# Performance work log

Hardware: AMD Instinct MI355X
Metric: run time of the kernel (lower is better)

The kernel has to match this reference:

```python
import jax, jax.numpy as jnp
import numpy as np

B, D_CAT, C_IN, C_OUT, K, H, W = 16, 512, 256, 256, 3, 64, 64


def setup_inputs() -> dict:
    key = jax.random.key(0)
    ks = jax.random.split(key, 9)
    inp = {
        "x": jax.random.normal(ks[0], (B, C_IN, H, W), dtype=jnp.float32),
        "y": jax.random.normal(ks[1], (B, D_CAT), dtype=jnp.float32),
        # EqualLinear stack: d_catin -> in_channels, then n_dl=2 layers in_channels -> in_channels
        "w0": jax.random.normal(ks[2], (C_IN, D_CAT), dtype=jnp.float32) / np.sqrt(D_CAT),
        "b0": jnp.zeros((C_IN,), dtype=jnp.float32),
        "w1": jax.random.normal(ks[3], (C_IN, C_IN), dtype=jnp.float32) / np.sqrt(C_IN),
        "b1": jnp.zeros((C_IN,), dtype=jnp.float32),
        "w2": jax.random.normal(ks[4], (C_IN, C_IN), dtype=jnp.float32) / np.sqrt(C_IN),
        "b2": jnp.zeros((C_IN,), dtype=jnp.float32),
        # shared conv weight (O, I, k, k), modulated per sample
        "conv_w": jax.random.normal(ks[5], (C_OUT, C_IN, K, K), dtype=jnp.float32) / np.sqrt(C_IN * K * K),
    }
    return inp


def _lrelu(z):
    # nn.LeakyReLU default negative_slope = 0.01
    return jnp.where(z >= 0, z, 0.01 * z)


def reference(x, y, w0, b0, w1, b1, w2, b2, conv_w):
    # style MLP (EqualLinear stack with LeakyReLU)
    s = _lrelu(y @ w0.T + b0)          # (B, C_in)
    s = _lrelu(s @ w1.T + b1)
    s = _lrelu(s @ w2.T + b2)
    # Per-sample weight modulation: conv(x[b], W * s[b, None, :, None, None]).
    # Since the scale is per input channel (no demodulation), this is exactly
    # equivalent to scaling the input channels and running one shared conv —
    # the fused form a custom kernel would use.
    x_mod = x * s[:, :, None, None]    # (B, C_in, H, W)
    out = jax.lax.conv_general_dilated(
        x_mod, conv_w,
        window_strides=(1, 1),
        padding=((1, 1), (1, 1)),
        dimension_numbers=("NCHW", "OIHW", "NCHW"),
    )  # (B, C_out, H, W); conv has bias=False in _DyConv
    return out
```

## Files before the change

### kernel.cpp

```cpp
#include <hip/hip_runtime.h>

typedef short bf16x8 __attribute__((ext_vector_type(8)));
typedef float f32x4 __attribute__((ext_vector_type(4)));
typedef unsigned short ushort8 __attribute__((ext_vector_type(8)));
typedef unsigned short ushort4v __attribute__((ext_vector_type(4)));

#define BATCH 16
#define DCAT 512
#define CIN 256
#define COUT 256
#define HH 64
#define WW 64
#define HP 66
#define WP 66
#define PLANE (HP * WP * 8)
#define AHALO 52224
#define BBUF 32768

__device__ __forceinline__ unsigned short f2bf(float f) {
  unsigned int u = __float_as_uint(f);
  unsigned int r = (u + 0x7fffu + ((u >> 16) & 1u)) >> 16;
  return (unsigned short)r;
}

template <int IN_DIM>
__global__ void __launch_bounds__(256) mlp_layer(const float* __restrict__ in,
                                                 const float* __restrict__ w,
                                                 const float* __restrict__ bias,
                                                 float* __restrict__ out) {
  int wid = threadIdx.x >> 6, lane = threadIdx.x & 63;
  int oidx = blockIdx.x * 4 + wid;
  int b = oidx >> 8, c = oidx & 255;
  const float* wr = w + (size_t)c * IN_DIM;
  const float* ir = in + (size_t)b * IN_DIM;
  float sum = 0.f;
#pragma unroll
  for (int d0 = 0; d0 < IN_DIM; d0 += 256) {
    f32x4 wv = *(const f32x4*)(wr + d0 + lane * 4);
    f32x4 iv = *(const f32x4*)(ir + d0 + lane * 4);
    sum += wv[0] * iv[0] + wv[1] * iv[1] + wv[2] * iv[2] + wv[3] * iv[3];
  }
#pragma unroll
  for (int off = 32; off; off >>= 1) sum += __shfl_xor(sum, off, 64);
  if (lane == 0) {
    float a = sum + bias[c];
    out[oidx] = a >= 0.f ? a : 0.01f * a;
  }
}

__global__ void __launch_bounds__(256) prep_all(const float* __restrict__ t1,
                                                const float* __restrict__ w2,
                                                const float* __restrict__ b2,
                                                const float* __restrict__ x,
                                                const float* __restrict__ cw,
                                                unsigned short* __restrict__ xpad,
                                                unsigned short* __restrict__ wt) {
  int blk = blockIdx.x;
  int tid = threadIdx.x;

  if (blk >= 1024) {
    int idx = (blk - 1024) * 256 + tid;
    int t = idx / 16384;
    int r = idx - t * 16384;
    int o = r >> 6, i4 = r & 63;
    ushort4v v;
#pragma unroll
    for (int j = 0; j < 4; j++) v[j] = f2bf(cw[(o * 256 + i4 * 4 + j) * 9 + t]);
    *(ushort4v*)(wt + ((size_t)(t * COUT + o)) * CIN + i4 * 4) = v;
    return;
  }

  int h = blk & 1, c8 = (blk >> 1) & 31, b = blk >> 6;
  int wid = tid >> 6, lane = tid & 63;

  float tv = t1[b * CIN + tid];
  float pj[8];
#pragma unroll
  for (int j = 0; j < 8; j++) pj[j] = w2[(size_t)(c8 * 8 + j) * CIN + tid] * tv;

  const float* xb = x + ((size_t)(b * CIN + c8 * 8)) * (HH * WW);
  int gg0 = h * 512 + tid;
  int gg1 = gg0 + 256;
  int hh0 = (gg0 >> 4) + 1, w00 = (gg0 & 15) * 4 + 1;
  int hh1 = (gg1 >> 4) + 1, w01 = (gg1 & 15) * 4 + 1;
  int base0 = (hh0 - 1) * WW + (w00 - 1);
  int base1 = (hh1 - 1) * WW + (w01 - 1);
  f32x4 v0[8], v1[8];
#pragma unroll
  for (int j = 0; j < 8; j++) v0[j] = *(const f32x4*)(xb + j * (HH * WW) + base0);
#pragma unroll
  for (int j = 0; j < 8; j++) v1[j] = *(const f32x4*)(xb + j * (HH * WW) + base1);

#pragma unroll
  for (int off = 32; off; off >>= 1)
#pragma unroll
    for (int j = 0; j < 8; j++) pj[j] += __shfl_xor(pj[j], off, 64);
  __shared__ float red[4][8];
  __shared__ float sv_sh[8];
  if (lane == 0)
#pragma unroll
    for (int j = 0; j < 8; j++) red[wid][j] = pj[j];
  __syncthreads();
  if (tid < 8) {
    float a = red[0][tid] + red[1][tid] + red[2][tid] + red[3][tid] + b2[c8 * 8 + tid];
    sv_sh[tid] = a >= 0.f ? a : 0.01f * a;
  }
  __syncthreads();
  float sv[8];
#pragma unroll
  for (int j = 0; j < 8; j++) sv[j] = sv_sh[j];

  unsigned short* xp = xpad + ((size_t)(b * 32 + c8)) * PLANE;

  if (tid < 130) {
    int i = h * 130 + tid;
    int bh, bw;
    if (i < 66) { bh = 0; bw = i; }
    else if (i < 132) { bh = 65; bw = i - 66; }
    else if (i < 196) { bh = i - 132 + 1; bw = 0; }
    else { bh = i - 196 + 1; bw = 65; }
    ushort8 z = {0, 0, 0, 0, 0, 0, 0, 0};
    *(ushort8*)(xp + (bh * WP + bw) * 8) = z;
  }

  unsigned short* op0 = xp + (hh0 * WP + w00) * 8;
  unsigned short* op1 = xp + (hh1 * WP + w01) * 8;
#pragma unroll
  for (int t2 = 0; t2 < 4; t2++) {
    ushort8 o;
#pragma unroll
    for (int j = 0; j < 8; j++) o[j] = f2bf(v0[j][t2] * sv[j]);
    *(ushort8*)(op0 + t2 * 8) = o;
  }
#pragma unroll
  for (int t2 = 0; t2 < 4; t2++) {
    ushort8 o;
#pragma unroll
    for (int j = 0; j < 8; j++) o[j] = f2bf(v1[j][t2] * sv[j]);
    *(ushort8*)(op1 + t2 * 8) = o;
  }
}

__device__ __forceinline__ void gl2lds16(const void* g, void* l) {
  __builtin_amdgcn_global_load_lds((const __attribute__((address_space(1))) void*)g,
                                   (__attribute__((address_space(3))) void*)l, 16, 0, 0);
}

__global__ void __launch_bounds__(512, 1) gemm_conv(const unsigned short* __restrict__ xpad,
                                                    const unsigned short* __restrict__ wt,
                                                    float* __restrict__ out) {
  __shared__ __align__(16) char lds[AHALO + 2 * BBUF];
  int tid = threadIdx.x;
  int wid = tid >> 6, lane = tid & 63;
  int bid = blockIdx.x;
  int m_t = (bid & 7) * 32 + (bid >> 3);
  int m0 = m_t << 8;
  int b = m0 >> 12;
  int h0 = (m0 >> 6) & 63;
  int wm = wid & 1, wn = wid >> 1;

  f32x4 acc[8][4];
#pragma unroll
  for (int mi = 0; mi < 8; mi++)
#pragma unroll
    for (int ni = 0; ni < 4; ni++) acc[mi][ni] = (f32x4){0.f, 0.f, 0.f, 0.f};

  const unsigned short* aSrc[7];
#pragma unroll
  for (int i = 0; i < 7; i++) {
    int c = (i * 8 + wid) * 64 + lane;
    int e = c >> 3, cs = c & 7;
    int gs = cs ^ (e & 7);
    int rh = e / 68, wc = e - rh * 68;
    aSrc[i] = xpad + ((size_t)((b * 32 + gs) * HP + (h0 + rh))) * (WP * 8) + wc * 8;
  }

  int o_l = tid >> 3;
  int csb = tid & 7;
  const unsigned short* bL = wt + o_l * CIN + ((csb ^ (o_l & 7)) * 8);

  int qa = lane >> 4;
  int l15 = lane & 15;
  int rB = wn * 64 + l15;
  int offB0 = rB * 128 + ((qa ^ (rB & 7)) * 16);
  int offB1 = rB * 128 + (((qa + 4) ^ (rB & 7)) * 16);

  int cur = 0;
  for (int kc2 = 0; kc2 < 4; kc2++) {
    size_t kofs = (size_t)kc2 * 8 * PLANE;
#pragma unroll
    for (int i = 0; i < 6; i++)
      gl2lds16(aSrc[i] + kofs, lds + (i * 8 + wid) * 1024);
    if (wid < 3) gl2lds16(aSrc[6] + kofs, lds + (48 + wid) * 1024);
    {
      const unsigned short* bG = bL + kc2 * 64;
      char* dB = lds + AHALO + cur * BBUF + wid * 1024;
#pragma unroll
      for (int q = 0; q < 4; q++) gl2lds16(bG + q * 64 * CIN, dB + q * 8192);
    }
    __syncthreads();

    for (int kh = 0; kh < 3; kh++) {
      for (int kw = 0; kw < 3; kw++) {
        int tap = kh * 3 + kw;
        if (tap < 8) {
          const unsigned short* bG = bL + (tap + 1) * (COUT * CIN) + kc2 * 64;
          char* dB = lds + AHALO + (cur ^ 1) * BBUF + wid * 1024;
#pragma unroll
          for (int q = 0; q < 4; q++) gl2lds16(bG + q * 64 * CIN, dB + q * 8192);
        }

        int eb = (wm * 2 + kh) * 68 + l15 + kw;
        int s0 = eb & 7, s1 = (eb + 4) & 7;
        int a00 = eb * 128 + ((qa ^ s0) * 16);
        int a01 = (eb + 68) * 128 + ((qa ^ s1) * 16);
        int a10 = eb * 128 + (((qa + 4) ^ s0) * 16);
        int a11 = (eb + 68) * 128 + (((qa + 4) ^ s1) * 16);
        const char* Bb = lds + AHALO + cur * BBUF;

#pragma unroll
        for (int kb = 0; kb < 2; kb++) {
          int oa0 = kb ? a10 : a00;
          int oa1 = kb ? a11 : a01;
          int ob = kb ? offB1 : offB0;
          bf16x8 av[8], bv[4];
#pragma unroll
          for (int mi = 0; mi < 4; mi++) {
            av[mi] = *(const bf16x8*)(lds + oa0 + mi * 2048);
            av[4 + mi] = *(const bf16x8*)(lds + oa1 + mi * 2048);
          }
#pragma unroll
          for (int ni = 0; ni < 4; ni++)
            bv[ni] = *(const bf16x8*)(Bb + ob + ni * 2048);
          __builtin_amdgcn_s_setprio(1);
#pragma unroll
          for (int mi = 0; mi < 8; mi++)
#pragma unroll
            for (int ni = 0; ni < 4; ni++)
              acc[mi][ni] = __builtin_amdgcn_mfma_f32_16x16x32_bf16(av[mi], bv[ni],
                                                                    acc[mi][ni], 0, 0, 0);
          __builtin_amdgcn_s_setprio(0);
        }

        __syncthreads();
        cur ^= 1;
      }
    }
  }

  int pixbase = m0 & 4095;
  int quad = lane >> 4;
  int col = lane & 15;
#pragma unroll
  for (int mi = 0; mi < 8; mi++) {
    int pm = pixbase + wm * 128 + mi * 16 + quad * 4;
#pragma unroll
    for (int ni = 0; ni < 4; ni++) {
      int on = wn * 64 + ni * 16 + col;
      float* op = out + ((size_t)(b * COUT + on) << 12) + pm;
      *(f32x4*)op = acc[mi][ni];
    }
  }
}

extern "C" void kernel_launch(void* const* d_in, const int* in_sizes, int n_in,
                              void* d_out, int out_size, void* d_ws, size_t ws_size,
                              hipStream_t stream) {
  const float* x = (const float*)d_in[0];
  const float* y = (const float*)d_in[1];
  const float* w0 = (const float*)d_in[2];
  const float* b0 = (const float*)d_in[3];
  const float* w1 = (const float*)d_in[4];
  const float* b1 = (const float*)d_in[5];
  const float* w2 = (const float*)d_in[6];
  const float* b2 = (const float*)d_in[7];
  const float* cw = (const float*)d_in[8];
  float* out = (float*)d_out;

  char* ws = (char*)d_ws;
  unsigned short* xpad = (unsigned short*)ws;
  unsigned short* wt = (unsigned short*)(ws + 35684352);
  float* t0 = (float*)(ws + 35684352 + 2359296);
  float* t1 = (float*)(ws + 35684352 + 2359296 + 16384);

  mlp_layer<DCAT><<<BATCH * CIN / 4, 256, 0, stream>>>(y, w0, b0, t0);
  mlp_layer<CIN><<<BATCH * CIN / 4, 256, 0, stream>>>(t0, w1, b1, t1);
  prep_all<<<1024 + 576, 256, 0, stream>>>(t1, w2, b2, x, cw, xpad, wt);
  gemm_conv<<<BATCH * HH * WW / 256, 512, 0, stream>>>(xpad, wt, out);
}
```

Baseline: 199.0 us.

## Prefetch next chunk's first weight tap and hoist all LDS fragment loads before MFMAs

The weight tile for tap 0 of the next input-channel chunk is now prefetched during the last tap of the current chunk, instead of being loaded synchronously at the start of each chunk. This removes an exposed global-to-LDS load before the barrier at chunk boundaries. Separately, both k-halves' A and B fragments are loaded from LDS up front, then all 64 MFMAs issue back to back, which lets LDS latency overlap with compute. The cost is higher VGPR pressure from the doubled fragment registers, which could lower occupancy or cause spills.

```diff
diff --git a/kernel.cpp b/kernel.cpp
--- a/kernel.cpp
+++ b/kernel.cpp
@@ -192,9 +192,9 @@
     for (int i = 0; i < 6; i++)
       gl2lds16(aSrc[i] + kofs, lds + (i * 8 + wid) * 1024);
     if (wid < 3) gl2lds16(aSrc[6] + kofs, lds + (48 + wid) * 1024);
-    {
-      const unsigned short* bG = bL + kc2 * 64;
-      char* dB = lds + AHALO + cur * BBUF + wid * 1024;
+    if (kc2 == 0) {
+      const unsigned short* bG = bL;
+      char* dB = lds + AHALO + wid * 1024;
 #pragma unroll
       for (int q = 0; q < 4; q++) gl2lds16(bG + q * 64 * CIN, dB + q * 8192);
     }
@@ -203,8 +203,10 @@
     for (int kh = 0; kh < 3; kh++) {
       for (int kw = 0; kw < 3; kw++) {
         int tap = kh * 3 + kw;
-        if (tap < 8) {
-          const unsigned short* bG = bL + (tap + 1) * (COUT * CIN) + kc2 * 64;
+        if (tap < 8 || kc2 < 3) {
+          const unsigned short* bG = (tap < 8)
+              ? bL + (tap + 1) * (COUT * CIN) + kc2 * 64
+              : bL + (kc2 + 1) * 64;
           char* dB = lds + AHALO + (cur ^ 1) * BBUF + wid * 1024;
 #pragma unroll
           for (int q = 0; q < 4; q++) gl2lds16(bG + q * 64 * CIN, dB + q * 8192);
@@ -218,29 +220,39 @@
         int a11 = (eb + 68) * 128 + (((qa + 4) ^ s1) * 16);
         const char* Bb = lds + AHALO + cur * BBUF;
 
-#pragma unroll
-        for (int kb = 0; kb < 2; kb++) {
-          int oa0 = kb ? a10 : a00;
-          int oa1 = kb ? a11 : a01;
-          int ob = kb ? offB1 : offB0;
-          bf16x8 av[8], bv[4];
-#pragma unroll
-          for (int mi = 0; mi < 4; mi++) {
-            av[mi] = *(const bf16x8*)(lds + oa0 + mi * 2048);
-            av[4 + mi] = *(const bf16x8*)(lds + oa1 + mi * 2048);
-          }
+        bf16x8 av[8], bv0[4], aw[8], bv1[4];
+#pragma unroll
+        for (int mi = 0; mi < 4; mi++) {
+          av[mi] = *(const bf16x8*)(lds + a00 + mi * 2048);
+          av[4 + mi] = *(const bf16x8*)(lds + a01 + mi * 2048);
+        }
+#pragma unroll
+        for (int ni = 0; ni < 4; ni++)
+          bv0[ni] = *(const bf16x8*)(Bb + offB0 + ni * 2048);
+
+#pragma unroll
+        for (int mi = 0; mi < 4; mi++) {
+          aw[mi] = *(const bf16x8*)(lds + a10 + mi * 2048);
+          aw[4 + mi] = *(const bf16x8*)(lds + a11 + mi * 2048);
+        }
+#pragma unroll
+        for (int ni = 0; ni < 4; ni++)
+          bv1[ni] = *(const bf16x8*)(Bb + offB1 + ni * 2048);
+
+        __builtin_amdgcn_s_setprio(1);
+#pragma unroll
+        for (int mi = 0; mi < 8; mi++)
 #pragma unroll
           for (int ni = 0; ni < 4; ni++)
-            bv[ni] = *(const bf16x8*)(Bb + ob + ni * 2048);
-          __builtin_amdgcn_s_setprio(1);
-#pragma unroll
-          for (int mi = 0; mi < 8; mi++)
-#pragma unroll
-            for (int ni = 0; ni < 4; ni++)
-              acc[mi][ni] = __builtin_amdgcn_mfma_f32_16x16x32_bf16(av[mi], bv[ni],
-                                                                    acc[mi][ni], 0, 0, 0);
-          __builtin_amdgcn_s_setprio(0);
-        }
+            acc[mi][ni] = __builtin_amdgcn_mfma_f32_16x16x32_bf16(av[mi], bv0[ni],
+                                                                  acc[mi][ni], 0, 0, 0);
+#pragma unroll
+        for (int mi = 0; mi < 8; mi++)
+#pragma unroll
+          for (int ni = 0; ni < 4; ni++)
+            acc[mi][ni] = __builtin_amdgcn_mfma_f32_16x16x32_bf16(aw[mi], bv1[ni],
+                                                                  acc[mi][ni], 0, 0, 0);
+        __builtin_amdgcn_s_setprio(0);
 
         __syncthreads();
         cur ^= 1;
```

Measured after the change: 241.1 us. +21.1%, slower.

## Double-buffer input halo per channel slice with per-wave private weight tiles

Applied to the files above, without the earlier changes.

Splits the channel reduction into 8 slices of 32 channels with a double-buffered A halo. The next slice's halo is prefetched during tap 7 of the current slice. Each wave now stages its own private B weight tile, so the per-tap block barrier is replaced by vmcnt waits, and only one barrier per slice remains. This aims to overlap global-to-LDS loads with MFMA work and cut synchronisation. The cost is more, smaller pipeline steps, a finer swizzle, and fragile hand-written vmcnt counts.

```diff
diff --git a/kernel.cpp b/kernel.cpp
--- a/kernel.cpp
+++ b/kernel.cpp
@@ -14,8 +14,8 @@
 #define HP 66
 #define WP 66
 #define PLANE (HP * WP * 8)
-#define AHALO 52224
-#define BBUF 32768
+#define ABUF 26624
+#define BBASE (2 * ABUF)
 
 __device__ __forceinline__ unsigned short f2bf(float f) {
   unsigned int u = __float_as_uint(f);
@@ -149,7 +149,7 @@
 __global__ void __launch_bounds__(512, 1) gemm_conv(const unsigned short* __restrict__ xpad,
                                                     const unsigned short* __restrict__ wt,
                                                     float* __restrict__ out) {
-  __shared__ __align__(16) char lds[AHALO + 2 * BBUF];
+  __shared__ __align__(16) char lds[BBASE + 8 * 8192];
   int tid = threadIdx.x;
   int wid = tid >> 6, lane = tid & 63;
   int bid = blockIdx.x;
@@ -165,85 +165,102 @@
 #pragma unroll
     for (int ni = 0; ni < 4; ni++) acc[mi][ni] = (f32x4){0.f, 0.f, 0.f, 0.f};
 
-  const unsigned short* aSrc[7];
-#pragma unroll
-  for (int i = 0; i < 7; i++) {
-    int c = (i * 8 + wid) * 64 + lane;
-    int e = c >> 3, cs = c & 7;
-    int gs = cs ^ (e & 7);
-    int rh = e / 68, wc = e - rh * 68;
-    aSrc[i] = xpad + ((size_t)((b * 32 + gs) * HP + (h0 + rh))) * (WP * 8) + wc * 8;
-  }
-
-  int o_l = tid >> 3;
-  int csb = tid & 7;
-  const unsigned short* bL = wt + o_l * CIN + ((csb ^ (o_l & 7)) * 8);
+  const unsigned short* aSrc[4];
+  {
+    int gsA = (lane & 3) ^ ((lane >> 3) & 3);
+#pragma unroll
+    for (int i = 0; i < 4; i++) {
+      int L = wid + i * 8;
+      int e = L * 16 + (lane >> 2);
+      int rh = e / 68, wc = e - rh * 68;
+      aSrc[i] = xpad + ((size_t)((b * 32 + gsA) * HP + (h0 + rh))) * (WP * 8) + wc * 8;
+    }
+  }
+
+  const unsigned short* bS0 =
+      wt + (size_t)(wn * 64 + (lane >> 2)) * CIN + ((lane & 3) ^ ((lane >> 3) & 3)) * 8;
+  char* myB = lds + BBASE + wid * 8192;
 
   int qa = lane >> 4;
   int l15 = lane & 15;
-  int rB = wn * 64 + l15;
-  int offB0 = rB * 128 + ((qa ^ (rB & 7)) * 16);
-  int offB1 = rB * 128 + (((qa + 4) ^ (rB & 7)) * 16);
-
-  int cur = 0;
-  for (int kc2 = 0; kc2 < 4; kc2++) {
-    size_t kofs = (size_t)kc2 * 8 * PLANE;
-#pragma unroll
-    for (int i = 0; i < 6; i++)
-      gl2lds16(aSrc[i] + kofs, lds + (i * 8 + wid) * 1024);
-    if (wid < 3) gl2lds16(aSrc[6] + kofs, lds + (48 + wid) * 1024);
-    {
-      const unsigned short* bG = bL + kc2 * 64;
-      char* dB = lds + AHALO + cur * BBUF + wid * 1024;
-#pragma unroll
-      for (int q = 0; q < 4; q++) gl2lds16(bG + q * 64 * CIN, dB + q * 8192);
-    }
-    __syncthreads();
-
+  int obr = l15 * 64 + ((qa ^ ((l15 >> 1) & 3)) * 16);
+
+#define STAGE_B(BUF, SRC)                                        \
+  do {                                                           \
+    char* dB_ = myB + (BUF) * 4096;                              \
+    const unsigned short* s_ = (SRC);                            \
+    _Pragma("unroll")                                            \
+    for (int g = 0; g < 4; g++)                                  \
+      gl2lds16(s_ + g * 16 * CIN, dB_ + g * 1024);               \
+  } while (0)
+
+#define STAGE_A(SL)                                              \
+  do {                                                           \
+    size_t ao_ = (size_t)(SL) * 4 * PLANE;                       \
+    char* dA_ = lds + ((SL) & 1) * ABUF;                         \
+    _Pragma("unroll")                                            \
+    for (int i = 0; i < 4; i++) {                                \
+      int L_ = wid + i * 8;                                      \
+      if (L_ < 26) gl2lds16(aSrc[i] + ao_, dA_ + L_ * 1024);     \
+    }                                                            \
+  } while (0)
+
+  STAGE_A(0);
+  STAGE_B(0, bS0);
+  asm volatile("s_waitcnt vmcnt(0)" ::: "memory");
+  __builtin_amdgcn_s_barrier();
+
+  int bcur = 0;
+  for (int slice = 0; slice < 8; slice++) {
+    const char* Ac = lds + (slice & 1) * ABUF;
     for (int kh = 0; kh < 3; kh++) {
       for (int kw = 0; kw < 3; kw++) {
-        int tap = kh * 3 + kw;
-        if (tap < 8) {
-          const unsigned short* bG = bL + (tap + 1) * (COUT * CIN) + kc2 * 64;
-          char* dB = lds + AHALO + (cur ^ 1) * BBUF + wid * 1024;
-#pragma unroll
-          for (int q = 0; q < 4; q++) gl2lds16(bG + q * 64 * CIN, dB + q * 8192);
+        int t = kh * 3 + kw;
+        if (t < 8) {
+          STAGE_B(bcur ^ 1, bS0 + (size_t)(t + 1) * (COUT * CIN) + slice * 32);
+        } else if (slice < 7) {
+          STAGE_B(bcur ^ 1, bS0 + (slice + 1) * 32);
         }
+        if (t == 7 && slice < 7) STAGE_A(slice + 1);
+
+        if (t < 8) {
+          asm volatile("s_waitcnt vmcnt(4)" ::: "memory");
+        } else if (slice < 7) {
+          asm volatile("s_waitcnt vmcnt(7)" ::: "memory");
+        } else {
+          asm volatile("s_waitcnt vmcnt(0)" ::: "memory");
+        }
 
         int eb = (wm * 2 + kh) * 68 + l15 + kw;
-        int s0 = eb & 7, s1 = (eb + 4) & 7;
-        int a00 = eb * 128 + ((qa ^ s0) * 16);
-        int a01 = (eb + 68) * 128 + ((qa ^ s1) * 16);
-        int a10 = eb * 128 + (((qa + 4) ^ s0) * 16);
-        int a11 = (eb + 68) * 128 + (((qa + 4) ^ s1) * 16);
-        const char* Bb = lds + AHALO + cur * BBUF;
-
-#pragma unroll
-        for (int kb = 0; kb < 2; kb++) {
-          int oa0 = kb ? a10 : a00;
-          int oa1 = kb ? a11 : a01;
-          int ob = kb ? offB1 : offB0;
-          bf16x8 av[8], bv[4];
-#pragma unroll
-          for (int mi = 0; mi < 4; mi++) {
-            av[mi] = *(const bf16x8*)(lds + oa0 + mi * 2048);
-            av[4 + mi] = *(const bf16x8*)(lds + oa1 + mi * 2048);
-          }
+        int e2 = eb + 68;
+        int a0 = eb * 64 + ((qa ^ ((eb >> 1) & 3)) * 16);
+        int a1 = e2 * 64 + ((qa ^ ((e2 >> 1) & 3)) * 16);
+        const char* Bb = myB + bcur * 4096;
+
+        bf16x8 av[8], bv[4];
+#pragma unroll
+        for (int mi = 0; mi < 4; mi++) {
+          av[mi] = *(const bf16x8*)(Ac + a0 + mi * 1024);
+          av[4 + mi] = *(const bf16x8*)(Ac + a1 + mi * 1024);
+        }
+#pragma unroll
+        for (int ni = 0; ni < 4; ni++)
+          bv[ni] = *(const bf16x8*)(Bb + obr + ni * 1024);
+
+        __builtin_amdgcn_s_setprio(1);
+#pragma unroll
+        for (int mi = 0; mi < 8; mi++)
 #pragma unroll
           for (int ni = 0; ni < 4; ni++)
-            bv[ni] = *(const bf16x8*)(Bb + ob + ni * 2048);
-          __builtin_amdgcn_s_setprio(1);
-#pragma unroll
-          for (int mi = 0; mi < 8; mi++)
-#pragma unroll
-            for (int ni = 0; ni < 4; ni++)
-              acc[mi][ni] = __builtin_amdgcn_mfma_f32_16x16x32_bf16(av[mi], bv[ni],
-                                                                    acc[mi][ni], 0, 0, 0);
-          __builtin_amdgcn_s_setprio(0);
+            acc[mi][ni] = __builtin_amdgcn_mfma_f32_16x16x32_bf16(av[mi], bv[ni],
+                                                                  acc[mi][ni], 0, 0, 0);
+        __builtin_amdgcn_s_setprio(0);
+
+        if (t == 8 && slice < 7) {
+          asm volatile("s_waitcnt vmcnt(0)" ::: "memory");
+          __builtin_amdgcn_s_barrier();
         }
-
-        __syncthreads();
-        cur ^= 1;
+        bcur ^= 1;
       }
     }
   }
```

New measurement: 213.1 us. 1.07x slower.

## Shrink conv GEMM tile to 128x128 with two workgroups per CU

Applied to the files above, without the earlier changes.

The implicit-GEMM conv moves from 512-thread workgroups covering 256 pixels by all 256 output channels to 256-thread workgroups covering 128 pixels (two image rows) by half the output channels, with two workgroups per CU. The A halo and B double buffers are resized to match. The next chunk's first weight tap is now prefetched during the last tap of the current chunk, and the A halo for the next chunk is loaded after compute instead of at the top of the loop. The aim is better latency hiding through more concurrent workgroups and fewer idle stalls. The cost is smaller tiles with less data reuse, so each pixel tile is loaded twice and the halo overhead per pixel grows.

```diff
diff --git a/kernel.cpp b/kernel.cpp
--- a/kernel.cpp
+++ b/kernel.cpp
@@ -14,8 +14,8 @@
 #define HP 66
 #define WP 66
 #define PLANE (HP * WP * 8)
-#define AHALO 52224
-#define BBUF 32768
+#define ABH 33792
+#define BB 16384
 
 __device__ __forceinline__ unsigned short f2bf(float f) {
   unsigned int u = __float_as_uint(f);
@@ -146,117 +146,130 @@
                                    (__attribute__((address_space(3))) void*)l, 16, 0, 0);
 }
 
-__global__ void __launch_bounds__(512, 1) gemm_conv(const unsigned short* __restrict__ xpad,
+__global__ void __launch_bounds__(256, 2) gemm_conv(const unsigned short* __restrict__ xpad,
                                                     const unsigned short* __restrict__ wt,
                                                     float* __restrict__ out) {
-  __shared__ __align__(16) char lds[AHALO + 2 * BBUF];
+  __shared__ __align__(16) char lds[ABH + 2 * BB];
   int tid = threadIdx.x;
   int wid = tid >> 6, lane = tid & 63;
   int bid = blockIdx.x;
-  int m_t = (bid & 7) * 32 + (bid >> 3);
-  int m0 = m_t << 8;
+  int wgid = (bid & 7) * 128 + (bid >> 3);
+  int m_t = wgid >> 1;
+  int oh = wgid & 1;
+  int m0 = m_t << 7;
   int b = m0 >> 12;
   int h0 = (m0 >> 6) & 63;
   int wm = wid & 1, wn = wid >> 1;
 
-  f32x4 acc[8][4];
-#pragma unroll
-  for (int mi = 0; mi < 8; mi++)
+  f32x4 acc[4][4];
+#pragma unroll
+  for (int mi = 0; mi < 4; mi++)
 #pragma unroll
     for (int ni = 0; ni < 4; ni++) acc[mi][ni] = (f32x4){0.f, 0.f, 0.f, 0.f};
 
-  const unsigned short* aSrc[7];
-#pragma unroll
-  for (int i = 0; i < 7; i++) {
-    int c = (i * 8 + wid) * 64 + lane;
-    int e = c >> 3, cs = c & 7;
-    int gs = cs ^ (e & 7);
-    int rh = e / 68, wc = e - rh * 68;
-    aSrc[i] = xpad + ((size_t)((b * 32 + gs) * HP + (h0 + rh))) * (WP * 8) + wc * 8;
-  }
-
-  int o_l = tid >> 3;
-  int csb = tid & 7;
-  const unsigned short* bL = wt + o_l * CIN + ((csb ^ (o_l & 7)) * 8);
+  int gsw = (tid & 7) ^ ((tid >> 3) & 7);
+  const unsigned short* aSrc[9];
+#pragma unroll
+  for (int i = 0; i < 9; i++) {
+    int e = i * 32 + (tid >> 3);
+    int rh = e / 66, wc = e - rh * 66;
+    aSrc[i] = xpad + ((size_t)((b * 32 + gsw) * HP + (h0 + rh))) * (WP * 8) + wc * 8;
+  }
+  const unsigned short* bS = wt + (size_t)(oh * 128 + (tid >> 3)) * CIN + gsw * 8;
 
   int qa = lane >> 4;
   int l15 = lane & 15;
-  int rB = wn * 64 + l15;
-  int offB0 = rB * 128 + ((qa ^ (rB & 7)) * 16);
-  int offB1 = rB * 128 + (((qa + 4) ^ (rB & 7)) * 16);
+  int orow = wn * 64 + l15;
+  int offB0 = orow * 128 + ((qa ^ (l15 & 7)) * 16);
+  int offB1 = orow * 128 + (((qa + 4) ^ (l15 & 7)) * 16);
+
+#define STAGE_A(KC2)                                                     \
+  do {                                                                   \
+    size_t ko_ = (size_t)(KC2) * 8 * PLANE;                              \
+    _Pragma("unroll")                                                    \
+    for (int i = 0; i < 8; i++)                                          \
+      gl2lds16(aSrc[i] + ko_, lds + i * 4096 + wid * 1024);              \
+    if (wid == 0) gl2lds16(aSrc[8] + ko_, lds + 32768);                  \
+  } while (0)
+
+#define STAGE_B(BUF, TAP, KC2)                                           \
+  do {                                                                   \
+    const unsigned short* s_ = bS + (size_t)(TAP) * (COUT * CIN) + (KC2) * 64; \
+    char* d_ = lds + ABH + (BUF) * BB + wid * 1024;                      \
+    _Pragma("unroll")                                                    \
+    for (int q = 0; q < 4; q++)                                          \
+      gl2lds16(s_ + q * 32 * CIN, d_ + q * 4096);                        \
+  } while (0)
+
+  STAGE_A(0);
+  STAGE_B(0, 0, 0);
+  asm volatile("s_waitcnt vmcnt(0)" ::: "memory");
+  __builtin_amdgcn_s_barrier();
 
   int cur = 0;
   for (int kc2 = 0; kc2 < 4; kc2++) {
-    size_t kofs = (size_t)kc2 * 8 * PLANE;
-#pragma unroll
-    for (int i = 0; i < 6; i++)
-      gl2lds16(aSrc[i] + kofs, lds + (i * 8 + wid) * 1024);
-    if (wid < 3) gl2lds16(aSrc[6] + kofs, lds + (48 + wid) * 1024);
-    {
-      const unsigned short* bG = bL + kc2 * 64;
-      char* dB = lds + AHALO + cur * BBUF + wid * 1024;
-#pragma unroll
-      for (int q = 0; q < 4; q++) gl2lds16(bG + q * 64 * CIN, dB + q * 8192);
-    }
-    __syncthreads();
-
     for (int kh = 0; kh < 3; kh++) {
       for (int kw = 0; kw < 3; kw++) {
         int tap = kh * 3 + kw;
         if (tap < 8) {
-          const unsigned short* bG = bL + (tap + 1) * (COUT * CIN) + kc2 * 64;
-          char* dB = lds + AHALO + (cur ^ 1) * BBUF + wid * 1024;
-#pragma unroll
-          for (int q = 0; q < 4; q++) gl2lds16(bG + q * 64 * CIN, dB + q * 8192);
+          STAGE_B(cur ^ 1, tap + 1, kc2);
+        } else if (kc2 < 3) {
+          STAGE_B(cur ^ 1, 0, kc2 + 1);
         }
 
-        int eb = (wm * 2 + kh) * 68 + l15 + kw;
-        int s0 = eb & 7, s1 = (eb + 4) & 7;
-        int a00 = eb * 128 + ((qa ^ s0) * 16);
-        int a01 = (eb + 68) * 128 + ((qa ^ s1) * 16);
-        int a10 = eb * 128 + (((qa + 4) ^ s0) * 16);
-        int a11 = (eb + 68) * 128 + (((qa + 4) ^ s1) * 16);
-        const char* Bb = lds + AHALO + cur * BBUF;
-
-#pragma unroll
-        for (int kb = 0; kb < 2; kb++) {
-          int oa0 = kb ? a10 : a00;
-          int oa1 = kb ? a11 : a01;
-          int ob = kb ? offB1 : offB0;
-          bf16x8 av[8], bv[4];
-#pragma unroll
-          for (int mi = 0; mi < 4; mi++) {
-            av[mi] = *(const bf16x8*)(lds + oa0 + mi * 2048);
-            av[4 + mi] = *(const bf16x8*)(lds + oa1 + mi * 2048);
-          }
+        int e0 = (wm + kh) * 66 + l15 + kw;
+        int s0 = e0 & 7;
+        int a00 = e0 * 128 + ((qa ^ s0) * 16);
+        int a10 = e0 * 128 + (((qa + 4) ^ s0) * 16);
+        const char* Bb = lds + ABH + cur * BB;
+
+        bf16x8 av[4], aw[4], bv[4], bw[4];
+#pragma unroll
+        for (int mi = 0; mi < 4; mi++) {
+          av[mi] = *(const bf16x8*)(lds + a00 + mi * 2048);
+          aw[mi] = *(const bf16x8*)(lds + a10 + mi * 2048);
+        }
+#pragma unroll
+        for (int ni = 0; ni < 4; ni++) {
+          bv[ni] = *(const bf16x8*)(Bb + offB0 + ni * 2048);
+          bw[ni] = *(const bf16x8*)(Bb + offB1 + ni * 2048);
+        }
+
+        __builtin_amdgcn_s_setprio(1);
+#pragma unroll
+        for (int mi = 0; mi < 4; mi++)
 #pragma unroll
           for (int ni = 0; ni < 4; ni++)
-            bv[ni] = *(const bf16x8*)(Bb + ob + ni * 2048);
-          __builtin_amdgcn_s_setprio(1);
-#pragma unroll
-          for (int mi = 0; mi < 8; mi++)
-#pragma unroll
-            for (int ni = 0; ni < 4; ni++)
-              acc[mi][ni] = __builtin_amdgcn_mfma_f32_16x16x32_bf16(av[mi], bv[ni],
-                                                                    acc[mi][ni], 0, 0, 0);
-          __builtin_amdgcn_s_setprio(0);
-        }
+            acc[mi][ni] = __builtin_amdgcn_mfma_f32_16x16x32_bf16(av[mi], bv[ni],
+                                                                  acc[mi][ni], 0, 0, 0);
+#pragma unroll
+        for (int mi = 0; mi < 4; mi++)
+#pragma unroll
+          for (int ni = 0; ni < 4; ni++)
+            acc[mi][ni] = __builtin_amdgcn_mfma_f32_16x16x32_bf16(aw[mi], bw[ni],
+                                                                  acc[mi][ni], 0, 0, 0);
+        __builtin_amdgcn_s_setprio(0);
 
         __syncthreads();
         cur ^= 1;
       }
     }
+    if (kc2 < 3) {
+      STAGE_A(kc2 + 1);
+      asm volatile("s_waitcnt vmcnt(0)" ::: "memory");
+      __builtin_amdgcn_s_barrier();
+    }
   }
 
   int pixbase = m0 & 4095;
   int quad = lane >> 4;
   int col = lane & 15;
 #pragma unroll
-  for (int mi = 0; mi < 8; mi++) {
-    int pm = pixbase + wm * 128 + mi * 16 + quad * 4;
+  for (int mi = 0; mi < 4; mi++) {
+    int pm = pixbase + wm * 64 + mi * 16 + quad * 4;
 #pragma unroll
     for (int ni = 0; ni < 4; ni++) {
-      int on = wn * 64 + ni * 16 + col;
+      int on = oh * 128 + wn * 64 + ni * 16 + col;
       float* op = out + ((size_t)(b * COUT + on) << 12) + pm;
       *(f32x4*)op = acc[mi][ni];
     }
@@ -286,5 +299,5 @@
   mlp_layer<DCAT><<<BATCH * CIN / 4, 256, 0, stream>>>(y, w0, b0, t0);
   mlp_layer<CIN><<<BATCH * CIN / 4, 256, 0, stream>>>(t0, w1, b1, t1);
   prep_all<<<1024 + 576, 256, 0, stream>>>(t1, w2, b2, x, cw, xpad, wt);
-  gemm_conv<<<BATCH * HH * WW / 256, 512, 0, stream>>>(xpad, wt, out);
-}
+  gemm_conv<<<BATCH * HH * WW / 128 * 2, 256, 0, stream>>>(xpad, wt, out);
+}
```

Measured after the change: 204.9 us. 1.03x slower.
